# Kernel tuning notes

Measured on AMD Instinct MI355X. Metric: run time of the kernel, lower is better.

## Reference

```python
import jax, jax.numpy as jnp
import numpy as np

TAU = 0.25
VTH = 1.0
RESET = 0.0


def setup_inputs() -> dict:
    key = jax.random.key(0)
    B, T, U = 64, 256, 1024
    inputs = jax.random.normal(key, (B, T, U), dtype=jnp.float32)
    return {"inputs": inputs}


def reference(inputs):
    # inputs: (B, T, U). LIF recurrence over time with threshold + soft reset.
    dt = inputs.dtype
    tau = jnp.asarray(TAU, dt)
    vth = jnp.asarray(VTH, dt)
    reset = jnp.asarray(RESET, dt)

    def step(v, x_t):
        v = tau * v + (1.0 - tau) * x_t          # leaky integrate
        s = (v > vth).astype(dt)                  # fire
        v = v - s * vth + s * reset               # reset fired neurons
        return v, s

    B, T, U = inputs.shape
    v0 = jnp.zeros((B, U), dtype=dt)
    xs = jnp.swapaxes(inputs, 0, 1)               # (T, B, U)
    _, spikes = jax.lax.scan(step, v0, xs)        # (T, B, U)
    return jnp.swapaxes(spikes, 0, 1)             # (B, T, U)
```

## Files before the change

### kernel.cpp

```cpp
#include <hip/hip_runtime.h>
#include <hip/hip_bf16.h>


constexpr int kB = 64;
constexpr int kT = 256;
constexpr int kU = 1024;
constexpr int kC = 16;

__global__ __launch_bounds__(256)
void lif_kernel(const float* __restrict__ x, float* __restrict__ out) {
    const int idx = blockIdx.x * blockDim.x + threadIdx.x;
    const int b = idx >> 10;
    const int u = idx & (kU - 1);

    const size_t base = (size_t)b * kT * kU + u;
    const float* __restrict__ xp = x + base;
    float* __restrict__ op = out + base;

    float buf[kC];
#pragma unroll
    for (int j = 0; j < kC; ++j)
        buf[j] = xp[(size_t)j * kU];

    float v = 0.0f;
    for (int c = 0; c < kT / kC - 1; ++c) {
        const int t0 = c * kC;
        float nbuf[kC];
#pragma unroll
        for (int j = 0; j < kC; ++j)
            nbuf[j] = xp[(size_t)(t0 + kC + j) * kU];
#pragma unroll
        for (int j = 0; j < kC; ++j) {
            const float a = __fmul_rn(0.25f, v);
            const float cc = __fmul_rn(0.75f, buf[j]);
            v = __fadd_rn(a, cc);
            const float s = (v > 1.0f) ? 1.0f : 0.0f;
            v = __fsub_rn(v, s);
            __builtin_nontemporal_store(s, &op[(size_t)(t0 + j) * kU]);
        }
#pragma unroll
        for (int j = 0; j < kC; ++j)
            buf[j] = nbuf[j];
    }
    const int t0 = kT - kC;
#pragma unroll
    for (int j = 0; j < kC; ++j) {
        const float a = __fmul_rn(0.25f, v);
        const float cc = __fmul_rn(0.75f, buf[j]);
        v = __fadd_rn(a, cc);
        const float s = (v > 1.0f) ? 1.0f : 0.0f;
        v = __fsub_rn(v, s);
        __builtin_nontemporal_store(s, &op[(size_t)(t0 + j) * kU]);
    }
}

extern "C" void kernel_launch(void* const* d_in, const int* in_sizes, int n_in,
                              void* d_out, int out_size, void* d_ws, size_t ws_size,
                              hipStream_t stream) {
    const float* x = (const float*)d_in[0];
    float* out = (float*)d_out;

    const int nthreads = kB * kU;
    const int block = 256;
    const int grid = nthreads / block;
    lif_kernel<<<grid, block, 0, stream>>>(x, out);
}
```

Measured before the change: 106.8 us.

## Vectorize LIF to two neurons per thread with triple-buffered prefetch

Each thread now handles two adjacent neurons using 8-byte float2 loads and nontemporal stores, which halves the thread count and doubles the bytes per memory instruction. The input is prefetched two chunks ahead in a three-slot register ring buffer, and the time loop is fully unrolled. Block size drops to 128, so the grid stays at 256 blocks. The aim is more memory-level parallelism per thread, but the larger register footprint may cut occupancy, and with only 32K threads there may be too few waves to hide latency.

```diff
diff --git a/kernel.cpp b/kernel.cpp
--- a/kernel.cpp
+++ b/kernel.cpp
@@ -1,56 +1,64 @@
 #include <hip/hip_runtime.h>
-#include <hip/hip_bf16.h>
 
 
-constexpr int kB = 64;
-constexpr int kT = 256;
-constexpr int kU = 1024;
-constexpr int kC = 16;
+typedef float f32x2 __attribute__((ext_vector_type(2)));
 
-__global__ __launch_bounds__(256)
+constexpr int kB  = 64;
+constexpr int kT  = 256;
+constexpr int kU  = 1024;
+constexpr int kU2 = kU / 2;
+constexpr int kC  = 16;
+constexpr int kNCH = kT / kC;
+
+__global__ __launch_bounds__(128)
 void lif_kernel(const float* __restrict__ x, float* __restrict__ out) {
     const int idx = blockIdx.x * blockDim.x + threadIdx.x;
-    const int b = idx >> 10;
-    const int u = idx & (kU - 1);
+    const int b   = idx >> 9;
+    const int u2  = idx & (kU2 - 1);
 
-    const size_t base = (size_t)b * kT * kU + u;
-    const float* __restrict__ xp = x + base;
-    float* __restrict__ op = out + base;
+    const size_t base2 = (size_t)b * kT * kU2 + u2;
+    const f32x2* __restrict__ xp = reinterpret_cast<const f32x2*>(x) + base2;
+    f32x2* __restrict__ op       = reinterpret_cast<f32x2*>(out) + base2;
 
-    float buf[kC];
+    f32x2 buf[3][kC];
+
 #pragma unroll
     for (int j = 0; j < kC; ++j)
-        buf[j] = xp[(size_t)j * kU];
+        buf[0][j] = xp[(size_t)j * kU2];
+#pragma unroll
+    for (int j = 0; j < kC; ++j)
+        buf[1][j] = xp[(size_t)(kC + j) * kU2];
 
-    float v = 0.0f;
-    for (int c = 0; c < kT / kC - 1; ++c) {
-        const int t0 = c * kC;
-        float nbuf[kC];
+    float v0 = 0.0f, v1 = 0.0f;
+
 #pragma unroll
-        for (int j = 0; j < kC; ++j)
-            nbuf[j] = xp[(size_t)(t0 + kC + j) * kU];
+    for (int c = 0; c < kNCH; ++c) {
+        if (c + 2 < kNCH) {
+#pragma unroll
+            for (int j = 0; j < kC; ++j)
+                buf[(c + 2) % 3][j] = xp[(size_t)((c + 2) * kC + j) * kU2];
+        }
 #pragma unroll
         for (int j = 0; j < kC; ++j) {
-            const float a = __fmul_rn(0.25f, v);
-            const float cc = __fmul_rn(0.75f, buf[j]);
-            v = __fadd_rn(a, cc);
-            const float s = (v > 1.0f) ? 1.0f : 0.0f;
-            v = __fsub_rn(v, s);
-            __builtin_nontemporal_store(s, &op[(size_t)(t0 + j) * kU]);
+            const f32x2 xx = buf[c % 3][j];
+
+            const float a0 = __fmul_rn(0.25f, v0);
+            const float m0 = __fmul_rn(0.75f, xx.x);
+            v0 = __fadd_rn(a0, m0);
+            const float s0 = (v0 > 1.0f) ? 1.0f : 0.0f;
+            v0 = __fsub_rn(v0, s0);
+
+            const float a1 = __fmul_rn(0.25f, v1);
+            const float m1 = __fmul_rn(0.75f, xx.y);
+            v1 = __fadd_rn(a1, m1);
+            const float s1 = (v1 > 1.0f) ? 1.0f : 0.0f;
+            v1 = __fsub_rn(v1, s1);
+
+            f32x2 s;
+            s.x = s0;
+            s.y = s1;
+            __builtin_nontemporal_store(s, &op[(size_t)(c * kC + j) * kU2]);
         }
-#pragma unroll
-        for (int j = 0; j < kC; ++j)
-            buf[j] = nbuf[j];
-    }
-    const int t0 = kT - kC;
-#pragma unroll
-    for (int j = 0; j < kC; ++j) {
-        const float a = __fmul_rn(0.25f, v);
-        const float cc = __fmul_rn(0.75f, buf[j]);
-        v = __fadd_rn(a, cc);
-        const float s = (v > 1.0f) ? 1.0f : 0.0f;
-        v = __fsub_rn(v, s);
-        __builtin_nontemporal_store(s, &op[(size_t)(t0 + j) * kU]);
     }
 }
 
@@ -60,8 +68,8 @@
     const float* x = (const float*)d_in[0];
     float* out = (float*)d_out;
 
-    const int nthreads = kB * kU;
-    const int block = 256;
+    const int nthreads = kB * kU2;
+    const int block = 128;
     const int grid = nthreads / block;
     lif_kernel<<<grid, block, 0, stream>>>(x, out);
 }
```

Measured after the change: 108.8 us. Within noise of the previous version (+1.9%).
